# Performance work log

Measured on AMD Instinct MI355X. Metric: run time of the kernel, lower is better.

## Reference

```python
import jax, jax.numpy as jnp
from jax import lax
import numpy as np

G, K = 8, 9  # deformable groups, 3x3 kernel taps


def conv1x1_bn_relu(x, W, scale, bias):
    # Conv2d 1x1 (no bias) + folded eval-mode BatchNorm (per-channel scale/bias) + ReLU
    y = jnp.einsum('bchw,oc->bohw', x, W)
    return jax.nn.relu(y * scale[None, :, None, None] + bias[None, :, None, None])


def dcn_v2(feat, offset_feat, W_om, b_om, W_dcn, b_dcn):
    # Modulated deformable conv v2, 3x3, stride 1, pad 1, dilation 1,
    # deformable_groups=G, extra_offset_mask: offsets/mask predicted from offset_feat.
    B, C, H, W_ = feat.shape
    Cg = C // G
    om = lax.conv_general_dilated(offset_feat, W_om, (1, 1), ((1, 1), (1, 1)))
    om = om + b_om[None, :, None, None]              # [B, 3*G*K, H, W]
    o1, o2, m = jnp.split(om, 3, axis=1)
    off_y = o1.reshape(B, G, K, H, W_)
    off_x = o2.reshape(B, G, K, H, W_)
    mask = jax.nn.sigmoid(m).reshape(B, G, K, H, W_)
    dk = jnp.arange(3) - 1
    dkh = jnp.repeat(dk, 3)   # tap row offset,  k = kh*3 + kw
    dkw = jnp.tile(dk, 3)     # tap col offset
    hh = jnp.arange(H, dtype=feat.dtype)
    ww = jnp.arange(W_, dtype=feat.dtype)
    py = hh[None, None, None, :, None] + dkh[None, None, :, None, None].astype(feat.dtype) + off_y
    px = ww[None, None, None, None, :] + dkw[None, None, :, None, None].astype(feat.dtype) + off_x
    y0 = jnp.floor(py); x0 = jnp.floor(px)
    ty = py - y0; tx = px - x0
    xg = feat.reshape(B, G, Cg, H * W_)

    def gather(idx):  # idx [B,G,K,H,W] int32 -> [B,G,Cg,K,H,W]
        f = lambda xf, i: xf[:, i]
        return jax.vmap(jax.vmap(f))(xg, idx)

    val = jnp.zeros((B, G, Cg, K, H, W_), dtype=feat.dtype)
    y0i = y0.astype(jnp.int32); x0i = x0.astype(jnp.int32)
    for dy, wy in ((0, 1.0 - ty), (1, ty)):
        iy = y0i + dy
        vy = (iy >= 0) & (iy < H)
        iyc = jnp.clip(iy, 0, H - 1)
        for dx, wx in ((0, 1.0 - tx), (1, tx)):
            ix = x0i + dx
            v = vy & (ix >= 0) & (ix < W_)
            idx = iyc * W_ + jnp.clip(ix, 0, W_ - 1)
            w = (wy * wx) * v.astype(feat.dtype)      # zero-padding outside
            val = val + w[:, :, None] * gather(idx)
    val = val * mask[:, :, None]                      # modulation
    Wd = W_dcn.reshape(W_dcn.shape[0], G, Cg, K)      # [Cout, G, Cg, K]
    out = jnp.einsum('bgckhw,ogck->bohw', val, Wd) + b_dcn[None, :, None, None]
    return out


def setup_inputs() -> dict:
    key = jax.random.key(0)
    ks = jax.random.split(key, 16)
    B, C, H, W_ = 8, 128, 64, 64
    Cd = C // 2  # dcn out channels = 64
    d = {}
    d['feat_l'] = jax.random.normal(ks[0], (B, C, H, W_), jnp.float32)
    d['feat_s'] = jax.random.normal(ks[1], (B, C, H // 2, W_ // 2), jnp.float32)
    d['W_fsm'] = jax.random.normal(ks[2], (C, C), jnp.float32) / np.sqrt(C)
    d['s_fsm'] = 1.0 + 0.1 * jax.random.normal(ks[3], (C,), jnp.float32)
    d['b_fsm'] = 0.1 * jax.random.normal(ks[4], (C,), jnp.float32)
    d['W_off'] = jax.random.normal(ks[5], (C, 2 * C), jnp.float32) / np.sqrt(2 * C)
    d['s_off'] = 1.0 + 0.1 * jax.random.normal(ks[6], (C,), jnp.float32)
    d['b_off'] = 0.1 * jax.random.normal(ks[7], (C,), jnp.float32)
    d['W_om'] = 0.05 * jax.random.normal(ks[8], (3 * G * K, C, 3, 3), jnp.float32)
    d['b_om'] = jnp.zeros((3 * G * K,), jnp.float32)
    d['W_dcn'] = jax.random.normal(ks[9], (Cd, C, 3, 3), jnp.float32) / np.sqrt(C * 9)
    d['b_dcn'] = 0.1 * jax.random.normal(ks[10], (Cd,), jnp.float32)
    d['W_cat'] = jax.random.normal(ks[11], (C, Cd), jnp.float32) / np.sqrt(Cd)
    d['s_cat'] = 1.0 + 0.1 * jax.random.normal(ks[12], (C,), jnp.float32)
    d['b_cat'] = 0.1 * jax.random.normal(ks[13], (C,), jnp.float32)
    return d


def reference(feat_l, feat_s, W_fsm, s_fsm, b_fsm, W_off, s_off, b_off,
              W_om, b_om, W_dcn, b_dcn, W_cat, s_cat, b_cat):
    # nearest upsample x2 (F.interpolate nearest to feat_l spatial size)
    feat_up = jnp.repeat(jnp.repeat(feat_s, 2, axis=2), 2, axis=3)
    feat_arm = conv1x1_bn_relu(feat_l, W_fsm, s_fsm, b_fsm)
    offset = conv1x1_bn_relu(jnp.concatenate([feat_arm, feat_up * 2.0], axis=1),
                             W_off, s_off, b_off)
    feat_align = jax.nn.relu(dcn_v2(feat_up, offset, W_om, b_om, W_dcn, b_dcn))
    feat = conv1x1_bn_relu(feat_align, W_cat, s_cat, b_cat) + feat_arm
    return (feat, feat_arm)
```

## Files before the change

kernel.cpp:

```cpp
#include <hip/hip_runtime.h>


typedef __attribute__((ext_vector_type(8))) short short8;
typedef __attribute__((ext_vector_type(4))) float f32x4;
typedef _Float16 __attribute__((ext_vector_type(2))) h2;

static __device__ __forceinline__ unsigned short f2bf(float x) {
    union { float f; unsigned int u; } v; v.f = x;
    return (unsigned short)((v.u + 0x7FFF + ((v.u >> 16) & 1)) >> 16);
}
static __device__ __forceinline__ unsigned short f2h(float x) {
    union { _Float16 h; unsigned short u; } v; v.h = (_Float16)x;
    return v.u;
}

__global__ __launch_bounds__(256) void k_prep(const float* __restrict__ fs,
        uint4* __restrict__ fsT4, uint4* __restrict__ fsC4,
        const float* __restrict__ W_fsm, const float* __restrict__ W_off,
        const float* __restrict__ W_cat, const float* __restrict__ W_dcn,
        const float* __restrict__ W_om,
        unsigned short* __restrict__ wbfsm, unsigned short* __restrict__ wboff,
        unsigned short* __restrict__ wbcat, unsigned short* __restrict__ wbdcn,
        unsigned short* __restrict__ wb2) {
    __shared__ unsigned short st[64 * 136];
    const int t = threadIdx.x;
    if (blockIdx.x < 128) {
        unsigned int* st32 = (unsigned int*)st;
        const int b = blockIdx.x >> 4;
        const int p0 = (blockIdx.x & 15) << 6;
        for (int i = t; i < 64 * 64; i += 256) {
            int c2 = i >> 6, px = i & 63;
            float v0 = fs[(((b << 7) + 2 * c2) << 10) + p0 + px];
            float v1 = fs[(((b << 7) + 2 * c2 + 1) << 10) + p0 + px];
            st32[px * 68 + c2] = (unsigned int)f2bf(v0) | ((unsigned int)f2bf(v1) << 16);
        }
        __syncthreads();
        for (int i = t; i < 64 * 16; i += 256) {
            int px = i >> 4, q = i & 15;
            fsT4[(((b << 10) + p0 + px) << 4) + q] = ((const uint4*)(st + px * 136))[q];
        }
        __syncthreads();
        for (int i = t; i < 64 * 64; i += 256) {
            int c2 = i >> 6, px = i & 63;
            float v0 = fs[(((b << 7) + 2 * c2) << 10) + p0 + px];
            float v1 = fs[(((b << 7) + 2 * c2 + 1) << 10) + p0 + px];
            st32[px * 68 + c2] = (unsigned int)f2h(v0) | ((unsigned int)f2h(v1) << 16);
        }
        __syncthreads();
        for (int i = t; i < 64 * 16; i += 256) {
            int ci = i >> 6, px = i & 63;
            fsC4[(b << 14) + (ci << 10) + p0 + px] = ((const uint4*)(st + px * 136))[ci];
        }
        return;
    }
    int idx = (blockIdx.x - 128) * 256 + t;
    int lane = idx & 63;
    int ml = lane & 15, kl = (lane >> 4) * 8;
    unsigned short tmp[8];
    if (idx < 2048) {
        int r = idx >> 6;
        int o = (r % 8) * 16 + ml, k0 = (r / 8) * 32 + kl;
#pragma unroll
        for (int j = 0; j < 8; j++) tmp[j] = f2bf(W_fsm[o * 128 + k0 + j]);
        ((uint4*)wbfsm)[idx] = *(const uint4*)tmp;
    } else if (idx < 6144) {
        int i2 = idx - 2048;
        int r = i2 >> 6;
        int o = (r % 8) * 16 + ml, k0 = (r / 8) * 32 + kl;
#pragma unroll
        for (int j = 0; j < 8; j++) {
            int k = k0 + j;
            float f = W_off[o * 256 + k];
            if (k >= 128) f *= 2.0f;
            tmp[j] = f2bf(f);
        }
        ((uint4*)wboff)[i2] = *(const uint4*)tmp;
    } else if (idx < 7168) {
        int i2 = idx - 6144;
        int r = i2 >> 6;
        int o = (r % 8) * 16 + ml, k0 = (r / 8) * 32 + kl;
#pragma unroll
        for (int j = 0; j < 8; j++) tmp[j] = f2bf(W_cat[o * 64 + k0 + j]);
        ((uint4*)wbcat)[i2] = *(const uint4*)tmp;
    } else if (idx < 16384) {
        int i2 = idx - 7168;
        int r = i2 >> 6;
        int o = (r & 3) * 16 + ml, k0 = (r >> 2) * 32 + kl;
#pragma unroll
        for (int j = 0; j < 8; j++) {
            int k = k0 + j;
            int g = k / 144;
            int rem = k - g * 144;
            tmp[j] = f2h(W_dcn[(o * 128 + g * 16 + (rem & 15)) * 9 + (rem >> 4)]);
        }
        ((uint4*)wbdcn)[i2] = *(const uint4*)tmp;
    } else if (idx < 53248) {
        int i2 = idx - 16384;
        int r = i2 >> 6;
        int nt = r & 15, kk = r >> 4;
        int tap = kk >> 2, cc = kk & 3;
        int o = nt * 16 + ml;
        int c0 = cc * 32 + kl;
#pragma unroll
        for (int j = 0; j < 8; j++) {
            float v = (o < 216) ? W_om[(o * 128 + (c0 + j)) * 9 + tap] : 0.0f;
            tmp[j] = f2bf(v);
        }
        ((uint4*)wb2)[i2] = *(const uint4*)tmp;
    }
}

__global__ __launch_bounds__(512, 4) void k12(const float* __restrict__ feat_l,
        const uint4* __restrict__ fsT4,
        const unsigned short* __restrict__ wbf, const unsigned short* __restrict__ wbo,
        const float* __restrict__ s_fsm, const float* __restrict__ b_fsm,
        const float* __restrict__ s_off, const float* __restrict__ b_off,
        float* __restrict__ feat_arm, unsigned short* __restrict__ offT) {
    __shared__ unsigned short A1[64 * 136];
    __shared__ unsigned short A2[64 * 264];
    float* E32 = (float*)A1;
    const int t = threadIdx.x;
    const int b = blockIdx.x >> 6;
    const int h = blockIdx.x & 63;
    const int hw0 = h << 6;
    unsigned int* A1w = (unsigned int*)A1;
    for (int i = t; i < 64 * 64; i += 512) {
        int c2 = i >> 6, px = i & 63;
        float v0 = feat_l[(((b << 7) + 2 * c2) << 12) + hw0 + px];
        float v1 = feat_l[(((b << 7) + 2 * c2 + 1) << 12) + hw0 + px];
        A1w[px * 68 + c2] = (unsigned int)f2bf(v0) | ((unsigned int)f2bf(v1) << 16);
    }
    {
        const int h2 = h >> 1;
        int px2 = t >> 4, q = t & 15;
        uint4 v = fsT4[(((b << 10) + (h2 << 5) + px2) << 4) + q];
        ((uint4*)(A2 + (2 * px2) * 264 + 128))[q] = v;
        ((uint4*)(A2 + (2 * px2 + 1) * 264 + 128))[q] = v;
    }
    __syncthreads();
    const int lane = t & 63;
    const int w = __builtin_amdgcn_readfirstlane(t >> 6);
    const int pq = w & 3;
    const int nh = w >> 2;
    const int m = lane & 15, ko = lane >> 4;
    f32x4 acc[4];
#pragma unroll
    for (int nt2 = 0; nt2 < 4; nt2++) acc[nt2] = (f32x4){0.f, 0.f, 0.f, 0.f};
#pragma unroll
    for (int kk = 0; kk < 4; kk++) {
        short8 av = *(const short8*)(A1 + (pq * 16 + m) * 136 + kk * 32 + ko * 8);
        const uint4* wb = (const uint4*)wbf + (kk * 8 + nh * 4) * 64 + lane;
#pragma unroll
        for (int nt2 = 0; nt2 < 4; nt2++) {
            uint4 bu = wb[nt2 * 64];
            acc[nt2] = __builtin_amdgcn_mfma_f32_16x16x32_bf16(av, *(short8*)&bu, acc[nt2], 0, 0, 0);
        }
    }
#pragma unroll
    for (int nt2 = 0; nt2 < 4; nt2++) {
        int o = ((nh << 2) + nt2) * 16 + m;
        float sc = s_fsm[o], bi = b_fsm[o];
#pragma unroll
        for (int r = 0; r < 4; r++) {
            float v = fmaf(acc[nt2][r], sc, bi);
            v = v > 0.f ? v : 0.f;
            acc[nt2][r] = v;
            A2[(pq * 16 + ko * 4 + r) * 264 + o] = f2bf(v);
        }
    }
#pragma unroll 1
    for (int half = 0; half < 2; half++) {
        __syncthreads();
        if (nh == half) {
#pragma unroll
            for (int nt2 = 0; nt2 < 4; nt2++)
#pragma unroll
                for (int r = 0; r < 4; r++)
                    E32[(pq * 16 + ko * 4 + r) * 67 + nt2 * 16 + m] = acc[nt2][r];
        }
        __syncthreads();
        for (int i = t; i < 4096; i += 512) {
            int ol = i >> 6, pp = i & 63;
            feat_arm[(((b << 7) + half * 64 + ol) << 12) + hw0 + pp] = E32[pp * 67 + ol];
        }
    }
    __syncthreads();
    f32x4 acc2[4];
#pragma unroll
    for (int nt2 = 0; nt2 < 4; nt2++) acc2[nt2] = (f32x4){0.f, 0.f, 0.f, 0.f};
#pragma unroll
    for (int kk = 0; kk < 8; kk++) {
        short8 av = *(const short8*)(A2 + (pq * 16 + m) * 264 + kk * 32 + ko * 8);
        const uint4* wb = (const uint4*)wbo + (kk * 8 + nh * 4) * 64 + lane;
#pragma unroll
        for (int nt2 = 0; nt2 < 4; nt2++) {
            uint4 bu = wb[nt2 * 64];
            acc2[nt2] = __builtin_amdgcn_mfma_f32_16x16x32_bf16(av, *(short8*)&bu, acc2[nt2], 0, 0, 0);
        }
    }
    __syncthreads();
#pragma unroll
    for (int nt2 = 0; nt2 < 4; nt2++) {
        int o = ((nh << 2) + nt2) * 16 + m;
        float sc = s_off[o], bi = b_off[o];
#pragma unroll
        for (int r = 0; r < 4; r++) {
            float v = fmaf(acc2[nt2][r], sc, bi);
            v = v > 0.f ? v : 0.f;
            A2[(pq * 16 + ko * 4 + r) * 264 + o] = f2bf(v);
        }
    }
    __syncthreads();
    for (int i = t; i < 64 * 16; i += 512) {
        int px = i >> 4, q = i & 15;
        ((uint4*)offT)[(((b << 12) + hw0 + px) << 4) + q] = ((const uint4*)(A2 + px * 264))[q];
    }
}

static __device__ __forceinline__ void dcn_prep(int kk, int ko, const float* omrow,
        float fh, float fw, const uint4* __restrict__ fsC4, int b14,
        uint4& c00, uint4& c01, uint4& c10, uint4& c11,
        float& w00, float& w01, float& w10, float& w11) {
    int k0 = (kk << 5) + (ko << 3);
    int g = k0 / 144;
    int rem = k0 - g * 144;
    int tap = rem >> 4;
    int c0 = rem & 15;
    int ch = g * 9 + tap;
    float oy = omrow[ch];
    float ox = omrow[72 + ch];
    float mmv = omrow[144 + ch];
    mmv = 1.0f / (1.0f + __expf(-mmv));
    float py = fh + (float)(tap / 3 - 1) + oy;
    float pxx = fw + (float)(tap % 3 - 1) + ox;
    float y0f = floorf(py), x0f = floorf(pxx);
    float tyf = py - y0f, txf = pxx - x0f;
    int y0i = (int)y0f, x0i = (int)x0f;
    int y1i = y0i + 1, x1i = x0i + 1;
    bool vy0 = (y0i >= 0) && (y0i < 64);
    bool vy1 = (y1i >= 0) && (y1i < 64);
    bool vx0 = (x0i >= 0) && (x0i < 64);
    bool vx1 = (x1i >= 0) && (x1i < 64);
    w00 = (vy0 && vx0) ? (1.0f - tyf) * (1.0f - txf) * mmv : 0.0f;
    w01 = (vy0 && vx1) ? (1.0f - tyf) * txf * mmv : 0.0f;
    w10 = (vy1 && vx0) ? tyf * (1.0f - txf) * mmv : 0.0f;
    w11 = (vy1 && vx1) ? tyf * txf * mmv : 0.0f;
    int yc0 = y0i < 0 ? 0 : (y0i > 63 ? 63 : y0i);
    int yc1 = y1i < 0 ? 0 : (y1i > 63 ? 63 : y1i);
    int xc0 = x0i < 0 ? 0 : (x0i > 63 ? 63 : x0i);
    int xc1 = x1i < 0 ? 0 : (x1i > 63 ? 63 : x1i);
    int row0 = (yc0 >> 1) << 5, row1 = (yc1 >> 1) << 5;
    int ci = g * 2 + (c0 >> 3);
    const uint4* base = fsC4 + b14 + (ci << 10);
    c00 = base[row0 + (xc0 >> 1)];
    c01 = base[row0 + (xc1 >> 1)];
    c10 = base[row1 + (xc0 >> 1)];
    c11 = base[row1 + (xc1 >> 1)];
}

static __device__ __forceinline__ void dcn_consume(int kk,
        const uint4& c00, const uint4& c01, const uint4& c10, const uint4& c11,
        float w00, float w01, float w10, float w11,
        const uint4* __restrict__ wbd4, int lane, f32x4* accd) {
    _Float16 h00 = (_Float16)w00, h01 = (_Float16)w01;
    _Float16 h10 = (_Float16)w10, h11 = (_Float16)w11;
    h2 W00 = (h2){h00, h00}, W01 = (h2){h01, h01};
    h2 W10 = (h2){h10, h10}, W11 = (h2){h11, h11};
    union { uint4 u; h2 h[4]; } U00, U01, U10, U11;
    U00.u = c00; U01.u = c01; U10.u = c10; U11.u = c11;
    union { short8 s; h2 h[4]; } av;
#pragma unroll
    for (int c = 0; c < 4; c++)
        av.h[c] = U00.h[c] * W00 + U01.h[c] * W01 + U10.h[c] * W10 + U11.h[c] * W11;
    const uint4* wb = wbd4 + (kk << 2) * 64 + lane;
#pragma unroll
    for (int nt = 0; nt < 4; nt++) {
        uint4 bu = wb[nt * 64];
        accd[nt] = __builtin_amdgcn_mfma_f32_16x16x32_f16(av.s, *(short8*)&bu, accd[nt], 0, 0, 0);
    }
}

__global__ __launch_bounds__(512, 4) void k_omdcn(
        const unsigned short* __restrict__ offT, const uint4* __restrict__ fsC4,
        const unsigned short* __restrict__ Wb2, const float* __restrict__ bom,
        const unsigned short* __restrict__ wbd, const float* __restrict__ bd,
        const unsigned short* __restrict__ wbc,
        const float* __restrict__ s_cat, const float* __restrict__ b_cat,
        const float* __restrict__ feat_arm, float* __restrict__ feat) {
    __shared__ float LDSf[16384];
    unsigned short* st = (unsigned short*)LDSf;
    float* omT = LDSf;
    float* Rbuf = LDSf;
    unsigned short* A3 = (unsigned short*)(LDSf + 13888);
    float* T = LDSf;
    const uint4* offT4 = (const uint4*)offT;
    const uint4* W4 = (const uint4*)Wb2;
    const uint4* wbd4 = (const uint4*)wbd;
    const int t = threadIdx.x;
    const int b = blockIdx.x >> 6;
    const int h = blockIdx.x & 63;
    for (int i = t; i < 3 * 66 * 16; i += 512) {
        int q = i & 15;
        int rp = i >> 4;
        int r = rp / 66, p = rp - r * 66;
        int gy = h + r - 1, gx = p - 1;
        uint4 v = make_uint4(0, 0, 0, 0);
        if (gy >= 0 && gy < 64 && gx >= 0 && gx < 64)
            v = offT4[((((b << 6) + gy) << 6) + gx) * 16 + q];
        ((uint4*)(st + rp * 136))[q] = v;
    }
    __syncthreads();
    const int lane = t & 63;
    const int w = __builtin_amdgcn_readfirstlane(t >> 6);
    const int nq = w & 3;
    const int kh = w >> 2;
    const int m = lane & 15, ko = lane >> 4;
    f32x4 acc[16];
#pragma unroll
    for (int i = 0; i < 16; i++) acc[i] = (f32x4){0.f, 0.f, 0.f, 0.f};
    {
        const int kk0 = kh * 18;
        uint4 b4[4];
#pragma unroll
        for (int nt2 = 0; nt2 < 4; nt2++)
            b4[nt2] = W4[(((kk0 << 4) + (nq << 2) + nt2) << 6) + lane];
#pragma unroll
        for (int kki = 0; kki < 18; kki++) {
            const int kk = kk0 + kki;
            const int tap = kk >> 2, cc = kk & 3;
            const int dy = tap / 3, dx = tap - dy * 3;
            uint4 b4n[4];
            if (kki < 17) {
#pragma unroll
                for (int nt2 = 0; nt2 < 4; nt2++)
                    b4n[nt2] = W4[((((kk + 1) << 4) + (nq << 2) + nt2) << 6) + lane];
            }
            short8 a8[4];
#pragma unroll
            for (int mt = 0; mt < 4; mt++) {
                int p = mt * 16 + m + dx;
                a8[mt] = *(const short8*)(st + (dy * 66 + p) * 136 + (cc << 5) + (ko << 3));
            }
#pragma unroll
            for (int nt2 = 0; nt2 < 4; nt2++)
#pragma unroll
                for (int mt = 0; mt < 4; mt++)
                    acc[nt2 * 4 + mt] = __builtin_amdgcn_mfma_f32_16x16x32_bf16(
                        a8[mt], *(short8*)&b4[nt2], acc[nt2 * 4 + mt], 0, 0, 0);
            if (kki < 17) {
#pragma unroll
                for (int nt2 = 0; nt2 < 4; nt2++) b4[nt2] = b4n[nt2];
            }
        }
    }
    __syncthreads();
    if (kh == 0) {
#pragma unroll
        for (int nt2 = 0; nt2 < 4; nt2++) {
            int o = ((nq << 2) + nt2) * 16 + m;
            if (o < 216) {
                float bv = bom[o];
#pragma unroll
                for (int mt = 0; mt < 4; mt++) {
                    f32x4 v = acc[nt2 * 4 + mt];
#pragma unroll
                    for (int r = 0; r < 4; r++)
                        omT[(mt * 16 + (ko << 2) + r) * 217 + o] = v[r] + bv;
                }
            }
        }
    }
    __syncthreads();
    if (kh == 1) {
#pragma unroll
        for (int nt2 = 0; nt2 < 4; nt2++) {
            int o = ((nq << 2) + nt2) * 16 + m;
            if (o < 216) {
#pragma unroll
                for (int mt = 0; mt < 4; mt++) {
                    f32x4 v = acc[nt2 * 4 + mt];
#pragma unroll
                    for (int r = 0; r < 4; r++)
                        omT[(mt * 16 + (ko << 2) + r) * 217 + o] += v[r];
                }
            }
        }
    }
    __syncthreads();
    const int px = (nq << 4) + m;
    const float fh = (float)h, fw = (float)px;
    const int b14 = b << 14;
    const float* omrow = omT + px * 217;
    f32x4 accd[4];
#pragma unroll
    for (int nt = 0; nt < 4; nt++) accd[nt] = (f32x4){0.f, 0.f, 0.f, 0.f};
    {
        const int dk0 = kh * 18;
#pragma unroll
        for (int kp = 0; kp < 9; kp++) {
            const int kkA = dk0 + 2 * kp;
            const int kkB = kkA + 1;
            uint4 a00, a01, a10, a11, e00, e01, e10, e11;
            float wa00, wa01, wa10, wa11, wb00, wb01, wb10, wb11;
            dcn_prep(kkA, ko, omrow, fh, fw, fsC4, b14,
                     a00, a01, a10, a11, wa00, wa01, wa10, wa11);
            dcn_prep(kkB, ko, omrow, fh, fw, fsC4, b14,
                     e00, e01, e10, e11, wb00, wb01, wb10, wb11);
            dcn_consume(kkA, a00, a01, a10, a11, wa00, wa01, wa10, wa11, wbd4, lane, accd);
            dcn_consume(kkB, e00, e01, e10, e11, wb00, wb01, wb10, wb11, wbd4, lane, accd);
        }
    }
    __syncthreads();
    if (kh == 1) {
#pragma unroll
        for (int nt = 0; nt < 4; nt++)
            *(f32x4*)(Rbuf + ((nq << 6) + lane) * 20 + (nt << 2)) = accd[nt];
    }
    __syncthreads();
    if (kh == 0) {
#pragma unroll
        for (int nt = 0; nt < 4; nt++)
            accd[nt] += *(const f32x4*)(Rbuf + ((nq << 6) + lane) * 20 + (nt << 2));
#pragma unroll
        for (int nt = 0; nt < 4; nt++) {
            int o = (nt << 4) + m;
            float bv = bd[o];
#pragma unroll
            for (int r = 0; r < 4; r++) {
                float v = accd[nt][r] + bv;
                v = v > 0.f ? v : 0.f;
                A3[((nq << 4) + (ko << 2) + r) * 72 + o] = f2bf(v);
            }
        }
    }
    __syncthreads();
    f32x4 acc2[4];
#pragma unroll
    for (int nt2 = 0; nt2 < 4; nt2++) acc2[nt2] = (f32x4){0.f, 0.f, 0.f, 0.f};
#pragma unroll
    for (int kk2 = 0; kk2 < 2; kk2++) {
        short8 av = *(const short8*)(A3 + ((nq << 4) + m) * 72 + kk2 * 32 + (ko << 3));
#pragma unroll
        for (int nt2 = 0; nt2 < 4; nt2++) {
            uint4 bu = ((const uint4*)wbc)[(kk2 * 8 + (kh << 2) + nt2) * 64 + lane];
            acc2[nt2] = __builtin_amdgcn_mfma_f32_16x16x32_bf16(av, *(short8*)&bu, acc2[nt2], 0, 0, 0);
        }
    }
#pragma unroll 1
    for (int half = 0; half < 2; half++) {
        __syncthreads();
        if (kh == half) {
#pragma unroll
            for (int nt2 = 0; nt2 < 4; nt2++) {
                int o = (((kh << 2) + nt2) << 4) + m;
                float sc = s_cat[o], bi = b_cat[o];
#pragma unroll
                for (int r = 0; r < 4; r++) {
                    float v = fmaf(acc2[nt2][r], sc, bi);
                    v = v > 0.f ? v : 0.f;
                    T[((nq << 4) + (ko << 2) + r) * 67 + (nt2 << 4) + m] = v;
                }
            }
        }
        __syncthreads();
        for (int i = t; i < 4096; i += 512) {
            int ol = i >> 6, pp = i & 63;
            int gidx = (((b << 7) + half * 64 + ol) << 12) + (h << 6) + pp;
            feat[gidx] = T[pp * 67 + ol] + feat_arm[gidx];
        }
    }
}

extern "C" void kernel_launch(void* const* d_in, const int* in_sizes, int n_in,
                              void* d_out, int out_size, void* d_ws, size_t ws_size,
                              hipStream_t stream) {
    const float* feat_l = (const float*)d_in[0];
    const float* feat_s = (const float*)d_in[1];
    const float* W_fsm  = (const float*)d_in[2];
    const float* s_fsm  = (const float*)d_in[3];
    const float* b_fsm  = (const float*)d_in[4];
    const float* W_off  = (const float*)d_in[5];
    const float* s_off  = (const float*)d_in[6];
    const float* b_off  = (const float*)d_in[7];
    const float* W_om   = (const float*)d_in[8];
    const float* b_om   = (const float*)d_in[9];
    const float* W_dcn  = (const float*)d_in[10];
    const float* b_dcn  = (const float*)d_in[11];
    const float* W_cat  = (const float*)d_in[12];
    const float* s_cat  = (const float*)d_in[13];
    const float* b_cat  = (const float*)d_in[14];

    float* feat     = (float*)d_out;
    float* feat_arm = feat + 4194304;

    float* ws = (float*)d_ws;
    unsigned short* offT = (unsigned short*)ws;
    uint4* fsT4  = (uint4*)(ws + 9175040);
    unsigned short* wb2   = (unsigned short*)(ws + 9699328);
    unsigned short* wbfsm = (unsigned short*)(ws + 9846784);
    unsigned short* wboff = (unsigned short*)(ws + 9854976);
    unsigned short* wbcat = (unsigned short*)(ws + 9871360);
    unsigned short* wbdcn = (unsigned short*)(ws + 9875456);
    uint4* fsC4  = (uint4*)(ws + 9912320);

    k_prep<<<336, 256, 0, stream>>>(feat_s, fsT4, fsC4, W_fsm, W_off, W_cat,
                                    W_dcn, W_om, wbfsm, wboff, wbcat, wbdcn, wb2);

    k12<<<512, 512, 0, stream>>>(feat_l, fsT4, wbfsm, wboff,
                                 s_fsm, b_fsm, s_off, b_off, feat_arm, offT);
    k_omdcn<<<512, 512, 0, stream>>>(offT, fsC4, wb2, b_om, wbdcn, b_dcn,
                                     wbcat, s_cat, b_cat, feat_arm, feat);
}
```

Baseline: 161.7 us.

## Direct vector stores, rebalance offset conv across waves, deepen DCN gather pipeline

Replaces the LDS transpose round-trips for the feat_arm and final feat outputs with direct 16-byte per-lane global stores and loads, dropping several barriers. Restructures the offset/mask conv in k_omdcn so each wave owns two output tiles over all 36 K-steps instead of splitting K across wave pairs, which removes the LDS reduction pass. Turns the DCN bilinear gather into a three-slot rotating software pipeline that prefetches two taps ahead. Adds s_setprio around MFMA groups and raises k12's launch-bounds occupancy hint. The trade-offs are more registers held for the prefetch slots and global stores with a per-lane stride rather than fully coalesced rows.

```diff
diff --git a/kernel.cpp b/kernel.cpp
--- a/kernel.cpp
+++ b/kernel.cpp
@@ -110,7 +110,7 @@
     }
 }
 
-__global__ __launch_bounds__(512, 4) void k12(const float* __restrict__ feat_l,
+__global__ __launch_bounds__(512, 6) void k12(const float* __restrict__ feat_l,
         const uint4* __restrict__ fsT4,
         const unsigned short* __restrict__ wbf, const unsigned short* __restrict__ wbo,
         const float* __restrict__ s_fsm, const float* __restrict__ b_fsm,
@@ -118,7 +118,6 @@
         float* __restrict__ feat_arm, unsigned short* __restrict__ offT) {
     __shared__ unsigned short A1[64 * 136];
     __shared__ unsigned short A2[64 * 264];
-    float* E32 = (float*)A1;
     const int t = threadIdx.x;
     const int b = blockIdx.x >> 6;
     const int h = blockIdx.x & 63;
@@ -156,32 +155,21 @@
             acc[nt2] = __builtin_amdgcn_mfma_f32_16x16x32_bf16(av, *(short8*)&bu, acc[nt2], 0, 0, 0);
         }
     }
-#pragma unroll
-    for (int nt2 = 0; nt2 < 4; nt2++) {
-        int o = ((nh << 2) + nt2) * 16 + m;
-        float sc = s_fsm[o], bi = b_fsm[o];
-#pragma unroll
-        for (int r = 0; r < 4; r++) {
-            float v = fmaf(acc[nt2][r], sc, bi);
-            v = v > 0.f ? v : 0.f;
-            acc[nt2][r] = v;
-            A2[(pq * 16 + ko * 4 + r) * 264 + o] = f2bf(v);
-        }
-    }
-#pragma unroll 1
-    for (int half = 0; half < 2; half++) {
-        __syncthreads();
-        if (nh == half) {
-#pragma unroll
-            for (int nt2 = 0; nt2 < 4; nt2++)
-#pragma unroll
-                for (int r = 0; r < 4; r++)
-                    E32[(pq * 16 + ko * 4 + r) * 67 + nt2 * 16 + m] = acc[nt2][r];
-        }
-        __syncthreads();
-        for (int i = t; i < 4096; i += 512) {
-            int ol = i >> 6, pp = i & 63;
-            feat_arm[(((b << 7) + half * 64 + ol) << 12) + hw0 + pp] = E32[pp * 67 + ol];
+    {
+        const int px0 = pq * 16 + (ko << 2);
+#pragma unroll
+        for (int nt2 = 0; nt2 < 4; nt2++) {
+            int o = ((nh << 2) + nt2) * 16 + m;
+            float sc = s_fsm[o], bi = b_fsm[o];
+            f32x4 v;
+#pragma unroll
+            for (int r = 0; r < 4; r++) {
+                float vv = fmaf(acc[nt2][r], sc, bi);
+                vv = vv > 0.f ? vv : 0.f;
+                v[r] = vv;
+                A2[(px0 + r) * 264 + o] = f2bf(vv);
+            }
+            *(f32x4*)(feat_arm + ((((b << 7) + o) << 12) + hw0 + px0)) = v;
         }
     }
     __syncthreads();
@@ -273,11 +261,13 @@
     for (int c = 0; c < 4; c++)
         av.h[c] = U00.h[c] * W00 + U01.h[c] * W01 + U10.h[c] * W10 + U11.h[c] * W11;
     const uint4* wb = wbd4 + (kk << 2) * 64 + lane;
+    __builtin_amdgcn_s_setprio(1);
 #pragma unroll
     for (int nt = 0; nt < 4; nt++) {
         uint4 bu = wb[nt * 64];
         accd[nt] = __builtin_amdgcn_mfma_f32_16x16x32_f16(av.s, *(short8*)&bu, accd[nt], 0, 0, 0);
     }
+    __builtin_amdgcn_s_setprio(0);
 }
 
 __global__ __launch_bounds__(512, 4) void k_omdcn(
@@ -292,7 +282,6 @@
     float* omT = LDSf;
     float* Rbuf = LDSf;
     unsigned short* A3 = (unsigned short*)(LDSf + 13888);
-    float* T = LDSf;
     const uint4* offT4 = (const uint4*)offT;
     const uint4* W4 = (const uint4*)Wb2;
     const uint4* wbd4 = (const uint4*)wbd;
@@ -312,28 +301,27 @@
     __syncthreads();
     const int lane = t & 63;
     const int w = __builtin_amdgcn_readfirstlane(t >> 6);
-    const int nq = w & 3;
-    const int kh = w >> 2;
     const int m = lane & 15, ko = lane >> 4;
-    f32x4 acc[16];
-#pragma unroll
-    for (int i = 0; i < 16; i++) acc[i] = (f32x4){0.f, 0.f, 0.f, 0.f};
+    f32x4 acc[2][4];
+#pragma unroll
+    for (int i = 0; i < 2; i++)
+#pragma unroll
+        for (int j = 0; j < 4; j++) acc[i][j] = (f32x4){0.f, 0.f, 0.f, 0.f};
     {
-        const int kk0 = kh * 18;
-        uint4 b4[4];
-#pragma unroll
-        for (int nt2 = 0; nt2 < 4; nt2++)
-            b4[nt2] = W4[(((kk0 << 4) + (nq << 2) + nt2) << 6) + lane];
-#pragma unroll
-        for (int kki = 0; kki < 18; kki++) {
-            const int kk = kk0 + kki;
+        const int ntb = w << 1;
+        uint4 b4c[2];
+#pragma unroll
+        for (int nt2 = 0; nt2 < 2; nt2++)
+            b4c[nt2] = W4[((ntb + nt2) << 6) + lane];
+#pragma unroll
+        for (int kk = 0; kk < 36; kk++) {
             const int tap = kk >> 2, cc = kk & 3;
             const int dy = tap / 3, dx = tap - dy * 3;
-            uint4 b4n[4];
-            if (kki < 17) {
-#pragma unroll
-                for (int nt2 = 0; nt2 < 4; nt2++)
-                    b4n[nt2] = W4[((((kk + 1) << 4) + (nq << 2) + nt2) << 6) + lane];
+            uint4 b4n[2];
+            if (kk < 35) {
+#pragma unroll
+                for (int nt2 = 0; nt2 < 2; nt2++)
+                    b4n[nt2] = W4[((((kk + 1) << 4) + ntb + nt2) << 6) + lane];
             }
             short8 a8[4];
 #pragma unroll
@@ -341,52 +329,38 @@
                 int p = mt * 16 + m + dx;
                 a8[mt] = *(const short8*)(st + (dy * 66 + p) * 136 + (cc << 5) + (ko << 3));
             }
-#pragma unroll
-            for (int nt2 = 0; nt2 < 4; nt2++)
+            __builtin_amdgcn_s_setprio(1);
+#pragma unroll
+            for (int nt2 = 0; nt2 < 2; nt2++)
 #pragma unroll
                 for (int mt = 0; mt < 4; mt++)
-                    acc[nt2 * 4 + mt] = __builtin_amdgcn_mfma_f32_16x16x32_bf16(
-                        a8[mt], *(short8*)&b4[nt2], acc[nt2 * 4 + mt], 0, 0, 0);
-            if (kki < 17) {
-#pragma unroll
-                for (int nt2 = 0; nt2 < 4; nt2++) b4[nt2] = b4n[nt2];
-            }
-        }
-    }
-    __syncthreads();
-    if (kh == 0) {
-#pragma unroll
-        for (int nt2 = 0; nt2 < 4; nt2++) {
-            int o = ((nq << 2) + nt2) * 16 + m;
-            if (o < 216) {
-                float bv = bom[o];
-#pragma unroll
-                for (int mt = 0; mt < 4; mt++) {
-                    f32x4 v = acc[nt2 * 4 + mt];
-#pragma unroll
-                    for (int r = 0; r < 4; r++)
-                        omT[(mt * 16 + (ko << 2) + r) * 217 + o] = v[r] + bv;
-                }
-            }
-        }
-    }
-    __syncthreads();
-    if (kh == 1) {
-#pragma unroll
-        for (int nt2 = 0; nt2 < 4; nt2++) {
-            int o = ((nq << 2) + nt2) * 16 + m;
-            if (o < 216) {
-#pragma unroll
-                for (int mt = 0; mt < 4; mt++) {
-                    f32x4 v = acc[nt2 * 4 + mt];
-#pragma unroll
-                    for (int r = 0; r < 4; r++)
-                        omT[(mt * 16 + (ko << 2) + r) * 217 + o] += v[r];
-                }
-            }
-        }
-    }
-    __syncthreads();
+                    acc[nt2][mt] = __builtin_amdgcn_mfma_f32_16x16x32_bf16(
+                        a8[mt], *(short8*)&b4c[nt2], acc[nt2][mt], 0, 0, 0);
+            __builtin_amdgcn_s_setprio(0);
+            if (kk < 35) {
+#pragma unroll
+                for (int nt2 = 0; nt2 < 2; nt2++) b4c[nt2] = b4n[nt2];
+            }
+        }
+    }
+    __syncthreads();
+#pragma unroll
+    for (int nt2 = 0; nt2 < 2; nt2++) {
+        int o = (((w << 1) + nt2) << 4) + m;
+        if (o < 216) {
+            float bv = bom[o];
+#pragma unroll
+            for (int mt = 0; mt < 4; mt++) {
+                f32x4 v = acc[nt2][mt];
+#pragma unroll
+                for (int r = 0; r < 4; r++)
+                    omT[(mt * 16 + (ko << 2) + r) * 217 + o] = v[r] + bv;
+            }
+        }
+    }
+    __syncthreads();
+    const int nq = w & 3;
+    const int kh = w >> 2;
     const int px = (nq << 4) + m;
     const float fh = (float)h, fw = (float)px;
     const int b14 = b << 14;
@@ -396,18 +370,23 @@
     for (int nt = 0; nt < 4; nt++) accd[nt] = (f32x4){0.f, 0.f, 0.f, 0.f};
     {
         const int dk0 = kh * 18;
-#pragma unroll
-        for (int kp = 0; kp < 9; kp++) {
-            const int kkA = dk0 + 2 * kp;
-            const int kkB = kkA + 1;
-            uint4 a00, a01, a10, a11, e00, e01, e10, e11;
-            float wa00, wa01, wa10, wa11, wb00, wb01, wb10, wb11;
-            dcn_prep(kkA, ko, omrow, fh, fw, fsC4, b14,
-                     a00, a01, a10, a11, wa00, wa01, wa10, wa11);
-            dcn_prep(kkB, ko, omrow, fh, fw, fsC4, b14,
-                     e00, e01, e10, e11, wb00, wb01, wb10, wb11);
-            dcn_consume(kkA, a00, a01, a10, a11, wa00, wa01, wa10, wa11, wbd4, lane, accd);
-            dcn_consume(kkB, e00, e01, e10, e11, wb00, wb01, wb10, wb11, wbd4, lane, accd);
+        uint4 s00[3], s01[3], s10[3], s11[3];
+        float t00[3], t01[3], t10[3], t11[3];
+#pragma unroll
+        for (int i = 0; i < 2; i++)
+            dcn_prep(dk0 + i, ko, omrow, fh, fw, fsC4, b14,
+                     s00[i], s01[i], s10[i], s11[i], t00[i], t01[i], t10[i], t11[i]);
+#pragma unroll
+        for (int kki = 0; kki < 18; kki++) {
+            const int sc_ = kki % 3;
+            if (kki < 16) {
+                const int sp = (kki + 2) % 3;
+                dcn_prep(dk0 + kki + 2, ko, omrow, fh, fw, fsC4, b14,
+                         s00[sp], s01[sp], s10[sp], s11[sp],
+                         t00[sp], t01[sp], t10[sp], t11[sp]);
+            }
+            dcn_consume(dk0 + kki, s00[sc_], s01[sc_], s10[sc_], s11[sc_],
+                        t00[sc_], t01[sc_], t10[sc_], t11[sc_], wbd4, lane, accd);
         }
     }
     __syncthreads();
@@ -446,27 +425,27 @@
             acc2[nt2] = __builtin_amdgcn_mfma_f32_16x16x32_bf16(av, *(short8*)&bu, acc2[nt2], 0, 0, 0);
         }
     }
-#pragma unroll 1
-    for (int half = 0; half < 2; half++) {
-        __syncthreads();
-        if (kh == half) {
-#pragma unroll
-            for (int nt2 = 0; nt2 < 4; nt2++) {
-                int o = (((kh << 2) + nt2) << 4) + m;
-                float sc = s_cat[o], bi = b_cat[o];
-#pragma unroll
-                for (int r = 0; r < 4; r++) {
-                    float v = fmaf(acc2[nt2][r], sc, bi);
-                    v = v > 0.f ? v : 0.f;
-                    T[((nq << 4) + (ko << 2) + r) * 67 + (nt2 << 4) + m] = v;
-                }
-            }
-        }
-        __syncthreads();
-        for (int i = t; i < 4096; i += 512) {
-            int ol = i >> 6, pp = i & 63;
-            int gidx = (((b << 7) + half * 64 + ol) << 12) + (h << 6) + pp;
-            feat[gidx] = T[pp * 67 + ol] + feat_arm[gidx];
+    {
+        const int px0 = (nq << 4) + (ko << 2);
+        const int base = (b << 19) + (h << 6) + px0;
+        f32x4 fa[4];
+#pragma unroll
+        for (int nt2 = 0; nt2 < 4; nt2++) {
+            int o = (((kh << 2) + nt2) << 4) + m;
+            fa[nt2] = *(const f32x4*)(feat_arm + base + (o << 12));
+        }
+#pragma unroll
+        for (int nt2 = 0; nt2 < 4; nt2++) {
+            int o = (((kh << 2) + nt2) << 4) + m;
+            float sc = s_cat[o], bi = b_cat[o];
+            f32x4 v;
+#pragma unroll
+            for (int r = 0; r < 4; r++) {
+                float vv = fmaf(acc2[nt2][r], sc, bi);
+                vv = vv > 0.f ? vv : 0.f;
+                v[r] = vv + fa[nt2][r];
+            }
+            *(f32x4*)(feat + base + (o << 12)) = v;
         }
     }
 }
```

Result: no change. 161.3 us (-0.2%).
